# Kernel optimization log

Measured on AMD Instinct MI355X. Metric: run time of the kernel, lower is better.

## Reference

```python
import jax, jax.numpy as jnp
import numpy as np

DIM = 768
N_HEAD = 12
HEAD_DIM = 64
INNER = N_HEAD * HEAD_DIM
SCALE = HEAD_DIM ** -0.5


def setup_inputs() -> dict:
    key = jax.random.key(0)
    ks = jax.random.split(key, 12)
    B, Sf, St = 4, 2048, 2048
    from_tensor = jax.random.normal(ks[0], (B, Sf, DIM), dtype=jnp.float32)
    to_tensor = jax.random.normal(ks[1], (B, St, DIM), dtype=jnp.float32)
    attention_mask = jax.random.randint(ks[2], (B, Sf, St), 0, 2, dtype=jnp.int32)
    # Dense layers: kernel ~ RandomNormal (stddev 0.05, keras default), bias zeros
    def kern(k, fan_in, fan_out):
        return 0.05 * jax.random.normal(k, (fan_in, fan_out), dtype=jnp.float32)
    return {
        "from_tensor": from_tensor,
        "to_tensor": to_tensor,
        "attention_mask": attention_mask,
        "Wq": kern(ks[3], DIM, INNER), "bq": jnp.zeros((INNER,), jnp.float32),
        "Wk": kern(ks[4], DIM, INNER), "bk": jnp.zeros((INNER,), jnp.float32),
        "Wv": kern(ks[5], DIM, INNER), "bv": jnp.zeros((INNER,), jnp.float32),
        "Wo": kern(ks[6], INNER, DIM), "bo": jnp.zeros((DIM,), jnp.float32),
    }


def reference(from_tensor, to_tensor, attention_mask, Wq, bq, Wk, bk, Wv, bv, Wo, bo):
    B, Sf, _ = from_tensor.shape
    St = to_tensor.shape[1]
    # projections -> [B, S, n_head, head_dim] -> [B, n_head, S, head_dim]
    def split_heads(x, S):
        return x.reshape(B, S, N_HEAD, HEAD_DIM).transpose(0, 2, 1, 3)
    q = split_heads(from_tensor @ Wq + bq, Sf) * SCALE
    k = split_heads(to_tensor @ Wk + bk, St)
    v = split_heads(to_tensor @ Wv + bv, St)
    # scores [B, H, Sf, St]
    scores = jnp.einsum('bhik,bhjk->bhij', q, k)
    adder = (1.0 - attention_mask.astype(jnp.float32)) * -10000.0
    scores = scores + adder[:, None, :, :]
    probs = jax.nn.softmax(scores, axis=-1)
    out = jnp.einsum('bhij,bhjk->bhik', probs, v)  # [B, H, Sf, Dh]
    out = out.transpose(0, 2, 1, 3).reshape(B, Sf, INNER)
    return out @ Wo + bo
```

## Files before the change

### kernel.cpp

```cpp
#include <hip/hip_runtime.h>
#include <stdint.h>

#define DIM 768
#define NH 12
#define HD 64
#define BSZ 4
#define SEQ 2048
#define MROWS (BSZ*SEQ)

typedef __attribute__((ext_vector_type(8))) short v8s;
typedef __attribute__((ext_vector_type(4))) float v4f;
typedef __attribute__((ext_vector_type(8))) _Float16 v8h;
typedef __attribute__((ext_vector_type(2))) __fp16 v2fp;

__device__ __forceinline__ uint16_t f2bf(float x) {
  union { float f; uint32_t u; } v; v.f = x;
  uint32_t r = v.u + 0x7fffu + ((v.u >> 16) & 1u);
  return (uint16_t)(r >> 16);
}

#if __has_builtin(__builtin_amdgcn_cvt_pk_bf16_f32)
typedef __attribute__((ext_vector_type(2))) __bf16 v2bf;
__device__ __forceinline__ uint32_t pack_bf16(float a, float b) {
  union { v2bf v; uint32_t u; } c;
  c.v = __builtin_amdgcn_cvt_pk_bf16_f32(a, b);
  return c.u;
}
#else
__device__ __forceinline__ uint32_t pack_bf16(float a, float b) {
  return (uint32_t)f2bf(a) | ((uint32_t)f2bf(b) << 16);
}
#endif

__device__ __forceinline__ uint32_t pack_f16(float a, float b) {
#if __has_builtin(__builtin_amdgcn_cvt_pkrtz)
  union { v2fp h; uint32_t u; } c;
  c.h = __builtin_amdgcn_cvt_pkrtz(a, b);
  return c.u;
#else
  union { _Float16 h[2]; uint32_t u; } c;
  c.h[0] = (_Float16)a; c.h[1] = (_Float16)b; return c.u;
#endif
}

__device__ __forceinline__ float fexp2(float x) {
#if __has_builtin(__builtin_amdgcn_exp2f)
  return __builtin_amdgcn_exp2f(x);
#else
  return exp2f(x);
#endif
}

__device__ __forceinline__ unsigned long long spread4(uint32_t c) {
  unsigned long long x = c & 0xFFFFu;
  x = (x | (x << 24)) & 0x000000FF000000FFull;
  x = (x | (x << 12)) & 0x000F000F000F000Full;
  x = (x | (x << 6))  & 0x0303030303030303ull;
  x = (x | (x << 3))  & 0x1111111111111111ull;
  return x;
}

__device__ __forceinline__ void gl16(const void* g, void* l) {
  __builtin_amdgcn_global_load_lds(
      (const __attribute__((address_space(1))) unsigned int*)g,
      (__attribute__((address_space(3))) unsigned int*)l, 16, 0, 0);
}

__device__ __forceinline__ void pipe_sync() {
  asm volatile("s_waitcnt vmcnt(0)" ::: "memory");
  __builtin_amdgcn_s_barrier();
  __builtin_amdgcn_sched_barrier(0);
}

#define CVT_BLKS  12288
#define WT_BLKS   2304
#define MASK_BLKS 16384
__global__ __launch_bounds__(256) void prepass_kernel(
    const float* __restrict__ from_t, const float* __restrict__ to_t,
    uint16_t* __restrict__ Xf, uint16_t* __restrict__ Xt,
    const float* __restrict__ Wq, const float* __restrict__ Wk,
    const float* __restrict__ Wv, const float* __restrict__ Wo,
    uint16_t* __restrict__ WT,
    const int* __restrict__ maski, unsigned long long* __restrict__ Mbits)
{
  __shared__ float tile[32][33];
  int blk = blockIdx.x, tid = threadIdx.x;
  if (blk < CVT_BLKS) {
    int n4 = MROWS * DIM / 4;
    int i = blk * 256 + tid;
    const float* src = (i < n4) ? from_t : to_t;
    uint16_t* dst = (i < n4) ? Xf : Xt;
    int j = (i < n4) ? i : i - n4;
    float4 v = ((const float4*)src)[j];
    uint2 o;
    o.x = pack_bf16(v.x, v.y);
    o.y = pack_bf16(v.z, v.w);
    ((uint2*)dst)[j] = o;
  } else if (blk < CVT_BLKS + WT_BLKS) {
    int r = blk - CVT_BLKS;
    int z = r / 576, rem = r - z * 576;
    int by = rem / 24, bx = rem - by * 24;
    const float* src = (z==0) ? Wq : (z==1) ? Wk : (z==2) ? Wv : Wo;
    uint16_t* dst = WT + (size_t)z * DIM * DIM;
    int tx = tid & 31, ty = tid >> 5;
    int x  = bx * 32 + tx;
    int y0 = by * 32;
    for (int jj = ty; jj < 32; jj += 8)
      tile[jj][tx] = src[(size_t)(y0 + jj) * DIM + x];
    __syncthreads();
    int xo = y0 + tx;
    for (int jj = ty; jj < 32; jj += 8)
      dst[(size_t)(bx * 32 + jj) * DIM + xo] = f2bf(tile[tx][jj]);
  } else {
    int gtid = (blk - CVT_BLKS - WT_BLKS) * 256 + tid;
    int g = gtid >> 6;
    int lane = tid & 63;
    int b   = g >> 14;
    int q   = (g >> 3) & 2047;
    int ktb = (g & 7) * 4;
    size_t base = ((size_t)b * SEQ + q) * SEQ + (size_t)ktb * 64;
    int4 m = *(const int4*)&maski[base + (lane >> 4) * 64 + (lane & 15) * 4];
    unsigned long long b0 = __ballot(m.x != 0);
    unsigned long long b1 = __ballot(m.y != 0);
    unsigned long long b2 = __ballot(m.z != 0);
    unsigned long long b3 = __ballot(m.w != 0);
    int qd = lane >> 4, sh = qd * 16;
    unsigned long long word =  spread4((uint32_t)(b0 >> sh))
                            | (spread4((uint32_t)(b1 >> sh)) << 1)
                            | (spread4((uint32_t)(b2 >> sh)) << 2)
                            | (spread4((uint32_t)(b3 >> sh)) << 3);
    if ((lane & 15) == 0)
      Mbits[((size_t)b * 32 + ktb + qd) * SEQ + q] = word;
  }
}

__global__ __launch_bounds__(256) void gemm_kernel(
    const uint16_t* __restrict__ Xf, const uint16_t* __restrict__ Xt,
    const uint16_t* __restrict__ WT,
    const float* __restrict__ bq, const float* __restrict__ bk,
    const float* __restrict__ bv,
    uint16_t* __restrict__ Qw, uint16_t* __restrict__ Kw, uint16_t* __restrict__ Vw)
{
  __shared__ alignas(16) uint16_t As[2][128 * 32];
  __shared__ alignas(16) uint16_t Bs[2][128 * 32];
  int mode = blockIdx.z;
  const uint16_t* A = (mode == 0) ? Xf : Xt;
  const uint16_t* W = WT + (size_t)mode * DIM * DIM;
  const float* bias = (mode == 0) ? bq : (mode == 1) ? bk : bv;

  int m0 = blockIdx.x * 128, n0 = blockIdx.y * 128;
  int tid = threadIdx.x;
  int wave = tid >> 6, lane = tid & 63, lr = lane & 15, quad = lane >> 4;
  int wm = (wave >> 1) * 64, wn = (wave & 1) * 64;

  int seg = (lane & 3) ^ ((lane >> 3) & 3);
  const uint16_t* agl = A + (size_t)(m0 + wave * 32 + (lane >> 2)) * DIM + seg * 8;
  const uint16_t* bgl = W + (size_t)(n0 + wave * 32 + (lane >> 2)) * DIM + seg * 8;
  int lb = wave * 1024;
  int ck = (lr >> 1) & 3;

  v4f acc[4][4];
  v4f vz = {0.f, 0.f, 0.f, 0.f};
  #pragma unroll
  for (int i = 0; i < 4; i++)
    #pragma unroll
    for (int j = 0; j < 4; j++) acc[i][j] = vz;

  gl16(agl,            &As[0][lb]);
  gl16(agl + 16 * DIM, &As[0][lb + 512]);
  gl16(bgl,            &Bs[0][lb]);
  gl16(bgl + 16 * DIM, &Bs[0][lb + 512]);
  pipe_sync();

  int cur = 0;
  const int NT = DIM / 32;
  for (int t = 0; t < NT; ++t) {
    if (t + 1 < NT) {
      int kn = (t + 1) * 32;
      gl16(agl + kn,            &As[cur ^ 1][lb]);
      gl16(agl + kn + 16 * DIM, &As[cur ^ 1][lb + 512]);
      gl16(bgl + kn,            &Bs[cur ^ 1][lb]);
      gl16(bgl + kn + 16 * DIM, &Bs[cur ^ 1][lb + 512]);
    }
    v8s af[4], bfr[4];
    #pragma unroll
    for (int i = 0; i < 4; i++)
      af[i] = *(const v8s*)&As[cur][(wm + i * 16 + lr) * 32 + ((quad ^ ck) << 3)];
    #pragma unroll
    for (int j = 0; j < 4; j++)
      bfr[j] = *(const v8s*)&Bs[cur][(wn + j * 16 + lr) * 32 + ((quad ^ ck) << 3)];
    #pragma unroll
    for (int i = 0; i < 4; i++)
      #pragma unroll
      for (int j = 0; j < 4; j++)
        acc[i][j] = __builtin_amdgcn_mfma_f32_16x16x32_bf16(af[i], bfr[j], acc[i][j], 0, 0, 0);
    if (t + 1 < NT) pipe_sync();
    cur ^= 1;
  }

  float bj[4];
  #pragma unroll
  for (int j = 0; j < 4; j++) bj[j] = bias[n0 + wn + j * 16 + lr];

  if (mode == 2) {
    #pragma unroll
    for (int i = 0; i < 4; i++) {
      int m = m0 + wm + i * 16 + quad * 4;
      int b = m >> 11, s0 = m & 2047;
      int kk0 = s0 & 63;
      int pos = (kk0 >> 5) * 32 + ((kk0 >> 2) & 3) * 8 + ((kk0 >> 4) & 1) * 4;
      int chunk = pos >> 3, off = pos & 7;
      #pragma unroll
      for (int j = 0; j < 4; j++) {
        int n = n0 + wn + j * 16 + lr;
        int h = n >> 6, d = n & 63;
        uint2 pk;
        pk.x = pack_f16(acc[i][j][0] + bj[j], acc[i][j][1] + bj[j]);
        pk.y = pack_f16(acc[i][j][2] + bj[j], acc[i][j][3] + bj[j]);
        int idx = (s0 & ~63) + ((chunk ^ (d & 7)) << 3) + off;
        *(uint2*)&Vw[((size_t)(b * NH + h) * HD + d) * SEQ + idx] = pk;
      }
    }
  } else {
    uint16_t* Dst = (mode == 0) ? Qw : Kw;
    float scale = (mode == 0) ? 0.18033688f : 1.0f;
    #pragma unroll
    for (int i = 0; i < 4; i++) {
      int m = m0 + wm + i * 16 + quad * 4;
      int b = m >> 11, s0 = m & 2047;
      #pragma unroll
      for (int j = 0; j < 4; j++) {
        int n = n0 + wn + j * 16 + lr;
        int h = n >> 6, d = n & 63;
        #pragma unroll
        for (int r = 0; r < 4; r++) {
          float v = (acc[i][j][r] + bj[j]) * scale;
          int s = s0 + r;
          int dd = (mode == 1) ? ((((d >> 3) ^ (s & 7)) << 3) + (d & 7)) : d;
          Dst[((size_t)(b * NH + h) * SEQ + s) * HD + dd] = f2bf(v);
        }
      }
    }
  }
}

__global__ __launch_bounds__(256) void gemm64_kernel(
    const uint16_t* __restrict__ AO, const uint16_t* __restrict__ WT,
    const float* __restrict__ bo, float* __restrict__ Out)
{
  __shared__ alignas(16) uint16_t As[2][64 * 32];
  __shared__ alignas(16) uint16_t Bs[2][128 * 32];
  const uint16_t* W = WT + (size_t)3 * DIM * DIM;

  int m0 = blockIdx.x * 64, n0 = blockIdx.y * 128;
  int tid = threadIdx.x;
  int wave = tid >> 6, lane = tid & 63, lr = lane & 15, quad = lane >> 4;
  int wm = (wave >> 1) * 32, wn = (wave & 1) * 64;

  int seg = (lane & 3) ^ ((lane >> 3) & 3);
  const uint16_t* agl = AO + (size_t)(m0 + wave * 16 + (lane >> 2)) * DIM + seg * 8;
  const uint16_t* bgl = W  + (size_t)(n0 + wave * 32 + (lane >> 2)) * DIM + seg * 8;
  int lba = wave * 512;
  int lbb = wave * 1024;
  int ck = (lr >> 1) & 3;

  v4f acc[2][4];
  v4f vz = {0.f, 0.f, 0.f, 0.f};
  #pragma unroll
  for (int i = 0; i < 2; i++)
    #pragma unroll
    for (int j = 0; j < 4; j++) acc[i][j] = vz;

  gl16(agl,            &As[0][lba]);
  gl16(bgl,            &Bs[0][lbb]);
  gl16(bgl + 16 * DIM, &Bs[0][lbb + 512]);
  pipe_sync();

  int cur = 0;
  const int NT = DIM / 32;
  for (int t = 0; t < NT; ++t) {
    if (t + 1 < NT) {
      int kn = (t + 1) * 32;
      gl16(agl + kn,            &As[cur ^ 1][lba]);
      gl16(bgl + kn,            &Bs[cur ^ 1][lbb]);
      gl16(bgl + kn + 16 * DIM, &Bs[cur ^ 1][lbb + 512]);
    }
    v8s af[2], bfr[4];
    #pragma unroll
    for (int i = 0; i < 2; i++)
      af[i] = *(const v8s*)&As[cur][(wm + i * 16 + lr) * 32 + ((quad ^ ck) << 3)];
    #pragma unroll
    for (int j = 0; j < 4; j++)
      bfr[j] = *(const v8s*)&Bs[cur][(wn + j * 16 + lr) * 32 + ((quad ^ ck) << 3)];
    #pragma unroll
    for (int i = 0; i < 2; i++)
      #pragma unroll
      for (int j = 0; j < 4; j++)
        acc[i][j] = __builtin_amdgcn_mfma_f32_16x16x32_bf16(af[i], bfr[j], acc[i][j], 0, 0, 0);
    if (t + 1 < NT) pipe_sync();
    cur ^= 1;
  }

  float bj[4];
  #pragma unroll
  for (int j = 0; j < 4; j++) bj[j] = bo[n0 + wn + j * 16 + lr];

  #pragma unroll
  for (int i = 0; i < 2; i++) {
    int m = m0 + wm + i * 16 + quad * 4;
    #pragma unroll
    for (int j = 0; j < 4; j++) {
      int n = n0 + wn + j * 16 + lr;
      #pragma unroll
      for (int r = 0; r < 4; r++)
        Out[(size_t)(m + r) * DIM + n] = acc[i][j][r] + bj[j];
    }
  }
}

__global__ __launch_bounds__(256, 3) void flash_kernel(
    const uint16_t* __restrict__ Qg, const uint16_t* __restrict__ Kg,
    const uint16_t* __restrict__ Vg, const unsigned long long* __restrict__ Mb,
    uint16_t* __restrict__ AO)
{
  __shared__ alignas(16) uint16_t Ks[2][64 * 64];
  __shared__ alignas(16) uint16_t Vs[2][64 * 64];

  int tid = threadIdx.x, wave = tid >> 6, lane = tid & 63, lr = lane & 15, quad = lane >> 4;

  int d = blockIdx.x + (blockIdx.y << 4);
  int nid = (d & 7) * 96 + (d >> 3);
  int bh = nid >> 4;
  int q0 = (nid & 15) * 128;
  int b = bh / NH, h = bh - b * NH;

  const uint16_t* Qp = Qg + (size_t)bh * SEQ * HD;
  const uint16_t* Kp = Kg + (size_t)bh * SEQ * HD;
  const uint16_t* Vp = Vg + (size_t)bh * HD * SEQ;
  int qg0 = q0 + wave * 32 + lr;
  int qg1 = qg0 + 16;
  const unsigned long long* Mp0 = Mb + (size_t)b * 32 * SEQ + qg0;
  const unsigned long long* Mp1 = Mp0 + 16;

  int swk = lr & 7, sh0 = quad * 4;

  v8s qf0a = *(const v8s*)&Qp[(size_t)qg0 * HD + quad * 8];
  v8s qf0b = *(const v8s*)&Qp[(size_t)qg0 * HD + 32 + quad * 8];
  v8s qf1a = *(const v8s*)&Qp[(size_t)qg1 * HD + quad * 8];
  v8s qf1b = *(const v8s*)&Qp[(size_t)qg1 * HD + 32 + quad * 8];

  const uint16_t* kgl = Kp + ((size_t)(wave * 16 + (lane >> 3)) * HD + (lane & 7) * 8);
  const uint16_t* vgl = Vp + ((size_t)(wave * 16 + (lane >> 3)) * SEQ + (lane & 7) * 8);
  int lb = wave * 1024;

  v8h ones;
  #pragma unroll
  for (int i = 0; i < 8; i++) ones[i] = (_Float16)1.0f;

  v4f acc0[4], acc1[4], lacc0, lacc1;
  v4f vz = {0.f, 0.f, 0.f, 0.f};
  v4f m8 = {-8.f, -8.f, -8.f, -8.f};
  #pragma unroll
  for (int dt = 0; dt < 4; dt++) { acc0[dt] = vz; acc1[dt] = vz; }
  lacc0 = vz; lacc1 = vz;

  gl16(kgl,                   &Ks[0][lb]);
  gl16(kgl + (size_t)8 * HD,  &Ks[0][lb + 512]);
  gl16(vgl,                   &Vs[0][lb]);
  gl16(vgl + (size_t)8 * SEQ, &Vs[0][lb + 512]);
  unsigned long long mw0_cur = Mp0[0];
  unsigned long long mw1_cur = Mp1[0];
  __syncthreads();

  int cur = 0;
  const int NT = SEQ / 64;
  for (int it = 0; it < NT; ++it) {
    unsigned long long mw0_next = 0, mw1_next = 0;
    if (it + 1 < NT) {
      int kn = (it + 1) * 64;
      gl16(kgl + (size_t)kn * HD,       &Ks[cur ^ 1][lb]);
      gl16(kgl + (size_t)(kn + 8) * HD, &Ks[cur ^ 1][lb + 512]);
      gl16(vgl + kn,                    &Vs[cur ^ 1][lb]);
      gl16(vgl + kn + (size_t)8 * SEQ,  &Vs[cur ^ 1][lb + 512]);
      mw0_next = Mp0[(size_t)(it + 1) * SEQ];
      mw1_next = Mp1[(size_t)(it + 1) * SEQ];
    }

    uint32_t m0lo = (uint32_t)mw0_cur, m0hi = (uint32_t)(mw0_cur >> 32);
    uint32_t m1lo = (uint32_t)mw1_cur, m1hi = (uint32_t)(mw1_cur >> 32);
    v8h pf0[2], pf1[2];
    #pragma unroll
    for (int p = 0; p < 2; p++) {
      v4f sA0 = m8, sB0 = m8, sA1 = m8, sB1 = m8;
      __builtin_amdgcn_s_setprio(1);
      {
        int rowb = ((2 * p) * 16 + lr) << 6;
        v8s kf0 = *(const v8s*)&Ks[cur][rowb + ((quad ^ swk) << 3)];
        v8s kf1 = *(const v8s*)&Ks[cur][rowb + (((quad + 4) ^ swk) << 3)];
        sA0 = __builtin_amdgcn_mfma_f32_16x16x32_bf16(kf0, qf0a, sA0, 0, 0, 0);
        sA0 = __builtin_amdgcn_mfma_f32_16x16x32_bf16(kf1, qf0b, sA0, 0, 0, 0);
        sA1 = __builtin_amdgcn_mfma_f32_16x16x32_bf16(kf0, qf1a, sA1, 0, 0, 0);
        sA1 = __builtin_amdgcn_mfma_f32_16x16x32_bf16(kf1, qf1b, sA1, 0, 0, 0);
      }
      {
        int rowb = ((2 * p + 1) * 16 + lr) << 6;
        v8s kf0 = *(const v8s*)&Ks[cur][rowb + ((quad ^ swk) << 3)];
        v8s kf1 = *(const v8s*)&Ks[cur][rowb + (((quad + 4) ^ swk) << 3)];
        sB0 = __builtin_amdgcn_mfma_f32_16x16x32_bf16(kf0, qf0a, sB0, 0, 0, 0);
        sB0 = __builtin_amdgcn_mfma_f32_16x16x32_bf16(kf1, qf0b, sB0, 0, 0, 0);
        sB1 = __builtin_amdgcn_mfma_f32_16x16x32_bf16(kf0, qf1a, sB1, 0, 0, 0);
        sB1 = __builtin_amdgcn_mfma_f32_16x16x32_bf16(kf1, qf1b, sB1, 0, 0, 0);
      }
      __builtin_amdgcn_s_setprio(0);
      uint32_t w0 = p ? m0hi : m0lo, w1 = p ? m1hi : m1lo;
      uint32_t a0 = (w0 >> sh0) & 15u, b0 = (w0 >> (sh0 + 16)) & 15u;
      uint32_t a1 = (w1 >> sh0) & 15u, b1 = (w1 >> (sh0 + 16)) & 15u;
      float p0[8], p1[8];
      #pragma unroll
      for (int r = 0; r < 4; r++) {
        float e0a = fexp2(sA0[r]), e0b = fexp2(sB0[r]);
        float e1a = fexp2(sA1[r]), e1b = fexp2(sB1[r]);
        p0[r]     = (a0 & (1u << r)) ? e0a : 0.0f;
        p0[4 + r] = (b0 & (1u << r)) ? e0b : 0.0f;
        p1[r]     = (a1 & (1u << r)) ? e1a : 0.0f;
        p1[4 + r] = (b1 & (1u << r)) ? e1b : 0.0f;
      }
      union { uint4 u; v8h h; } c0, c1;
      c0.u.x = pack_f16(p0[0], p0[1]); c0.u.y = pack_f16(p0[2], p0[3]);
      c0.u.z = pack_f16(p0[4], p0[5]); c0.u.w = pack_f16(p0[6], p0[7]);
      c1.u.x = pack_f16(p1[0], p1[1]); c1.u.y = pack_f16(p1[2], p1[3]);
      c1.u.z = pack_f16(p1[4], p1[5]); c1.u.w = pack_f16(p1[6], p1[7]);
      pf0[p] = c0.h;
      pf1[p] = c1.h;
    }

    __builtin_amdgcn_s_setprio(1);
    #pragma unroll
    for (int dt = 0; dt < 4; dt++) {
      int rowb = (dt * 16 + lr) << 6;
      #pragma unroll
      for (int p = 0; p < 2; p++) {
        v8h vv = *(const v8h*)&Vs[cur][rowb + (((p * 4 + quad) ^ swk) << 3)];
        acc0[dt] = __builtin_amdgcn_mfma_f32_16x16x32_f16(vv, pf0[p], acc0[dt], 0, 0, 0);
        acc1[dt] = __builtin_amdgcn_mfma_f32_16x16x32_f16(vv, pf1[p], acc1[dt], 0, 0, 0);
      }
    }
    lacc0 = __builtin_amdgcn_mfma_f32_16x16x32_f16(ones, pf0[0], lacc0, 0, 0, 0);
    lacc0 = __builtin_amdgcn_mfma_f32_16x16x32_f16(ones, pf0[1], lacc0, 0, 0, 0);
    lacc1 = __builtin_amdgcn_mfma_f32_16x16x32_f16(ones, pf1[0], lacc1, 0, 0, 0);
    lacc1 = __builtin_amdgcn_mfma_f32_16x16x32_f16(ones, pf1[1], lacc1, 0, 0, 0);
    __builtin_amdgcn_s_setprio(0);

    __syncthreads();
    mw0_cur = mw0_next;
    mw1_cur = mw1_next;
    cur ^= 1;
  }

  float ri0 = 1.0f / lacc0[0];
  float ri1 = 1.0f / lacc1[0];

  #pragma unroll
  for (int dt = 0; dt < 4; dt++) {
    uint2 pk;
    pk.x = pack_bf16(acc0[dt][0] * ri0, acc0[dt][1] * ri0);
    pk.y = pack_bf16(acc0[dt][2] * ri0, acc0[dt][3] * ri0);
    *(uint2*)&AO[(size_t)(b * SEQ + qg0) * DIM + h * HD + dt * 16 + sh0] = pk;
    pk.x = pack_bf16(acc1[dt][0] * ri1, acc1[dt][1] * ri1);
    pk.y = pack_bf16(acc1[dt][2] * ri1, acc1[dt][3] * ri1);
    *(uint2*)&AO[(size_t)(b * SEQ + qg1) * DIM + h * HD + dt * 16 + sh0] = pk;
  }
}

extern "C" void kernel_launch(void* const* d_in, const int* in_sizes, int n_in,
                              void* d_out, int out_size, void* d_ws, size_t ws_size,
                              hipStream_t stream) {
  const float* from_t = (const float*)d_in[0];
  const float* to_t   = (const float*)d_in[1];
  const int*   maski  = (const int*)d_in[2];
  const float* Wq = (const float*)d_in[3];  const float* bq = (const float*)d_in[4];
  const float* Wk = (const float*)d_in[5];  const float* bk = (const float*)d_in[6];
  const float* Wv = (const float*)d_in[7];  const float* bv = (const float*)d_in[8];
  const float* Wo = (const float*)d_in[9];  const float* bo = (const float*)d_in[10];

  char* ws = (char*)d_ws;
  size_t off = 0;
  uint16_t* Xf = (uint16_t*)(ws + off); off += (size_t)MROWS * DIM * 2;
  uint16_t* Xt = (uint16_t*)(ws + off); off += (size_t)MROWS * DIM * 2;
  uint16_t* WT = (uint16_t*)(ws + off); off += (size_t)4 * DIM * DIM * 2;
  unsigned long long* Mbits = (unsigned long long*)(ws + off);
  off += (size_t)BSZ * 32 * SEQ * 8;
  uint16_t* Qw = (uint16_t*)(ws + off); off += (size_t)MROWS * DIM * 2;
  uint16_t* Kw = (uint16_t*)(ws + off); off += (size_t)MROWS * DIM * 2;
  uint16_t* Vw = (uint16_t*)(ws + off); off += (size_t)MROWS * DIM * 2;
  uint16_t* AO = (uint16_t*)(ws + off); off += (size_t)MROWS * DIM * 2;
  float* Out = (float*)d_out;

  prepass_kernel<<<CVT_BLKS + WT_BLKS + MASK_BLKS, 256, 0, stream>>>(
      from_t, to_t, Xf, Xt, Wq, Wk, Wv, Wo, WT, maski, Mbits);

  gemm_kernel<<<dim3(64, 6, 3), 256, 0, stream>>>(Xf, Xt, WT, bq, bk, bv,
                                                  Qw, Kw, Vw);
  flash_kernel<<<dim3(SEQ / 128, BSZ * NH), 256, 0, stream>>>(Qw, Kw, Vw, Mbits, AO);
  gemm64_kernel<<<dim3(128, 6), 256, 0, stream>>>(AO, WT, bo, Out);
}
```

Measured before the change: 304.6 us.

## Triple-buffer K/V tiles with prefetch distance two and manual vmcnt waits

Moves the flash attention loop from double to triple LDS buffering: each iteration issues async loads for the tile two steps ahead, waits with explicit s_waitcnt vmcnt(6) plus a raw s_barrier instead of __syncthreads, and unrolls by two so the mask words rotate between registers. The aim is to hide global load latency behind more compute and remove the full drain at each barrier. LDS per block grows from 32KB to 48KB, which may limit the three blocks per CU requested in launch bounds. The manual vmcnt counting also depends on exactly which memory ops are in flight.

```diff
diff --git a/kernel.cpp b/kernel.cpp
--- a/kernel.cpp
+++ b/kernel.cpp
@@ -318,13 +318,90 @@
   }
 }
 
+#define FLASH_TILE(CUR, M0LO, M0HI, M1LO, M1HI)                                   \
+  {                                                                               \
+    v8h pf0[2], pf1[2];                                                           \
+    _Pragma("unroll")                                                             \
+    for (int p = 0; p < 2; p++) {                                                 \
+      v4f sA0 = m8, sB0 = m8, sA1 = m8, sB1 = m8;                                 \
+      __builtin_amdgcn_s_setprio(1);                                              \
+      {                                                                           \
+        int rowb = ((2 * p) * 16 + lr) << 6;                                      \
+        v8s kf0 = *(const v8s*)&Ks[CUR][rowb + ((quad ^ swk) << 3)];              \
+        v8s kf1 = *(const v8s*)&Ks[CUR][rowb + (((quad + 4) ^ swk) << 3)];        \
+        sA0 = __builtin_amdgcn_mfma_f32_16x16x32_bf16(kf0, qf0a, sA0, 0, 0, 0);   \
+        sA0 = __builtin_amdgcn_mfma_f32_16x16x32_bf16(kf1, qf0b, sA0, 0, 0, 0);   \
+        sA1 = __builtin_amdgcn_mfma_f32_16x16x32_bf16(kf0, qf1a, sA1, 0, 0, 0);   \
+        sA1 = __builtin_amdgcn_mfma_f32_16x16x32_bf16(kf1, qf1b, sA1, 0, 0, 0);   \
+      }                                                                           \
+      {                                                                           \
+        int rowb = ((2 * p + 1) * 16 + lr) << 6;                                  \
+        v8s kf0 = *(const v8s*)&Ks[CUR][rowb + ((quad ^ swk) << 3)];              \
+        v8s kf1 = *(const v8s*)&Ks[CUR][rowb + (((quad + 4) ^ swk) << 3)];        \
+        sB0 = __builtin_amdgcn_mfma_f32_16x16x32_bf16(kf0, qf0a, sB0, 0, 0, 0);   \
+        sB0 = __builtin_amdgcn_mfma_f32_16x16x32_bf16(kf1, qf0b, sB0, 0, 0, 0);   \
+        sB1 = __builtin_amdgcn_mfma_f32_16x16x32_bf16(kf0, qf1a, sB1, 0, 0, 0);   \
+        sB1 = __builtin_amdgcn_mfma_f32_16x16x32_bf16(kf1, qf1b, sB1, 0, 0, 0);   \
+      }                                                                           \
+      __builtin_amdgcn_s_setprio(0);                                              \
+      uint32_t w0 = p ? (M0HI) : (M0LO), w1 = p ? (M1HI) : (M1LO);                \
+      uint32_t a0 = (w0 >> sh0) & 15u, b0 = (w0 >> (sh0 + 16)) & 15u;             \
+      uint32_t a1 = (w1 >> sh0) & 15u, b1 = (w1 >> (sh0 + 16)) & 15u;             \
+      float p0[8], p1[8];                                                         \
+      _Pragma("unroll")                                                           \
+      for (int r = 0; r < 4; r++) {                                               \
+        float e0a = fexp2(sA0[r]), e0b = fexp2(sB0[r]);                           \
+        float e1a = fexp2(sA1[r]), e1b = fexp2(sB1[r]);                           \
+        p0[r]     = (a0 & (1u << r)) ? e0a : 0.0f;                                \
+        p0[4 + r] = (b0 & (1u << r)) ? e0b : 0.0f;                                \
+        p1[r]     = (a1 & (1u << r)) ? e1a : 0.0f;                                \
+        p1[4 + r] = (b1 & (1u << r)) ? e1b : 0.0f;                                \
+      }                                                                           \
+      union { uint4 u; v8h h; } c0, c1;                                           \
+      c0.u.x = pack_f16(p0[0], p0[1]); c0.u.y = pack_f16(p0[2], p0[3]);           \
+      c0.u.z = pack_f16(p0[4], p0[5]); c0.u.w = pack_f16(p0[6], p0[7]);           \
+      c1.u.x = pack_f16(p1[0], p1[1]); c1.u.y = pack_f16(p1[2], p1[3]);           \
+      c1.u.z = pack_f16(p1[4], p1[5]); c1.u.w = pack_f16(p1[6], p1[7]);           \
+      pf0[p] = c0.h;                                                              \
+      pf1[p] = c1.h;                                                              \
+    }                                                                             \
+    __builtin_amdgcn_s_setprio(1);                                                \
+    _Pragma("unroll")                                                             \
+    for (int dt = 0; dt < 4; dt++) {                                              \
+      int rowb = (dt * 16 + lr) << 6;                                             \
+      _Pragma("unroll")                                                           \
+      for (int p = 0; p < 2; p++) {                                               \
+        v8h vv = *(const v8h*)&Vs[CUR][rowb + (((p * 4 + quad) ^ swk) << 3)];     \
+        acc0[dt] = __builtin_amdgcn_mfma_f32_16x16x32_f16(vv, pf0[p], acc0[dt], 0, 0, 0); \
+        acc1[dt] = __builtin_amdgcn_mfma_f32_16x16x32_f16(vv, pf1[p], acc1[dt], 0, 0, 0); \
+      }                                                                           \
+    }                                                                             \
+    lacc0 = __builtin_amdgcn_mfma_f32_16x16x32_f16(ones, pf0[0], lacc0, 0, 0, 0); \
+    lacc0 = __builtin_amdgcn_mfma_f32_16x16x32_f16(ones, pf0[1], lacc0, 0, 0, 0); \
+    lacc1 = __builtin_amdgcn_mfma_f32_16x16x32_f16(ones, pf1[0], lacc1, 0, 0, 0); \
+    lacc1 = __builtin_amdgcn_mfma_f32_16x16x32_f16(ones, pf1[1], lacc1, 0, 0, 0); \
+    __builtin_amdgcn_s_setprio(0);                                                \
+  }
+
+#define FLASH_STAGE(T, MW0, MW1)                                                  \
+  if ((T) + 2 < NT) {                                                             \
+    MW0 = Mp0[(size_t)((T) + 2) * SEQ];                                           \
+    MW1 = Mp1[(size_t)((T) + 2) * SEQ];                                           \
+    int kn = ((T) + 2) * 64;                                                      \
+    int nb = (cur == 0) ? 2 : cur - 1;                             \
+    gl16(kgl + (size_t)kn * HD,       &Ks[nb][lb]);                               \
+    gl16(kgl + (size_t)(kn + 8) * HD, &Ks[nb][lb + 512]);                         \
+    gl16(vgl + kn,                    &Vs[nb][lb]);                               \
+    gl16(vgl + kn + (size_t)8 * SEQ,  &Vs[nb][lb + 512]);                         \
+  }
+
 __global__ __launch_bounds__(256, 3) void flash_kernel(
     const uint16_t* __restrict__ Qg, const uint16_t* __restrict__ Kg,
     const uint16_t* __restrict__ Vg, const unsigned long long* __restrict__ Mb,
     uint16_t* __restrict__ AO)
 {
-  __shared__ alignas(16) uint16_t Ks[2][64 * 64];
-  __shared__ alignas(16) uint16_t Vs[2][64 * 64];
+  __shared__ alignas(16) uint16_t Ks[3][64 * 64];
+  __shared__ alignas(16) uint16_t Vs[3][64 * 64];
 
   int tid = threadIdx.x, wave = tid >> 6, lane = tid & 63, lr = lane & 15, quad = lane >> 4;
 
@@ -364,97 +441,46 @@
   for (int dt = 0; dt < 4; dt++) { acc0[dt] = vz; acc1[dt] = vz; }
   lacc0 = vz; lacc1 = vz;
 
-  gl16(kgl,                   &Ks[0][lb]);
-  gl16(kgl + (size_t)8 * HD,  &Ks[0][lb + 512]);
-  gl16(vgl,                   &Vs[0][lb]);
-  gl16(vgl + (size_t)8 * SEQ, &Vs[0][lb + 512]);
-  unsigned long long mw0_cur = Mp0[0];
-  unsigned long long mw1_cur = Mp1[0];
-  __syncthreads();
+  const int NT = SEQ / 64;
+
+  unsigned long long mwA0 = Mp0[0];
+  unsigned long long mwA1 = Mp1[0];
+  gl16(kgl,                    &Ks[0][lb]);
+  gl16(kgl + (size_t)8 * HD,   &Ks[0][lb + 512]);
+  gl16(vgl,                    &Vs[0][lb]);
+  gl16(vgl + (size_t)8 * SEQ,  &Vs[0][lb + 512]);
+  __builtin_amdgcn_sched_barrier(0);
+  unsigned long long mwB0 = Mp0[SEQ];
+  unsigned long long mwB1 = Mp1[SEQ];
+  gl16(kgl + (size_t)64 * HD,       &Ks[1][lb]);
+  gl16(kgl + (size_t)(64 + 8) * HD, &Ks[1][lb + 512]);
+  gl16(vgl + 64,                    &Vs[1][lb]);
+  gl16(vgl + 64 + (size_t)8 * SEQ,  &Vs[1][lb + 512]);
+  __builtin_amdgcn_sched_barrier(0);
 
   int cur = 0;
-  const int NT = SEQ / 64;
-  for (int it = 0; it < NT; ++it) {
-    unsigned long long mw0_next = 0, mw1_next = 0;
-    if (it + 1 < NT) {
-      int kn = (it + 1) * 64;
-      gl16(kgl + (size_t)kn * HD,       &Ks[cur ^ 1][lb]);
-      gl16(kgl + (size_t)(kn + 8) * HD, &Ks[cur ^ 1][lb + 512]);
-      gl16(vgl + kn,                    &Vs[cur ^ 1][lb]);
-      gl16(vgl + kn + (size_t)8 * SEQ,  &Vs[cur ^ 1][lb + 512]);
-      mw0_next = Mp0[(size_t)(it + 1) * SEQ];
-      mw1_next = Mp1[(size_t)(it + 1) * SEQ];
-    }
-
-    uint32_t m0lo = (uint32_t)mw0_cur, m0hi = (uint32_t)(mw0_cur >> 32);
-    uint32_t m1lo = (uint32_t)mw1_cur, m1hi = (uint32_t)(mw1_cur >> 32);
-    v8h pf0[2], pf1[2];
-    #pragma unroll
-    for (int p = 0; p < 2; p++) {
-      v4f sA0 = m8, sB0 = m8, sA1 = m8, sB1 = m8;
-      __builtin_amdgcn_s_setprio(1);
-      {
-        int rowb = ((2 * p) * 16 + lr) << 6;
-        v8s kf0 = *(const v8s*)&Ks[cur][rowb + ((quad ^ swk) << 3)];
-        v8s kf1 = *(const v8s*)&Ks[cur][rowb + (((quad + 4) ^ swk) << 3)];
-        sA0 = __builtin_amdgcn_mfma_f32_16x16x32_bf16(kf0, qf0a, sA0, 0, 0, 0);
-        sA0 = __builtin_amdgcn_mfma_f32_16x16x32_bf16(kf1, qf0b, sA0, 0, 0, 0);
-        sA1 = __builtin_amdgcn_mfma_f32_16x16x32_bf16(kf0, qf1a, sA1, 0, 0, 0);
-        sA1 = __builtin_amdgcn_mfma_f32_16x16x32_bf16(kf1, qf1b, sA1, 0, 0, 0);
-      }
-      {
-        int rowb = ((2 * p + 1) * 16 + lr) << 6;
-        v8s kf0 = *(const v8s*)&Ks[cur][rowb + ((quad ^ swk) << 3)];
-        v8s kf1 = *(const v8s*)&Ks[cur][rowb + (((quad + 4) ^ swk) << 3)];
-        sB0 = __builtin_amdgcn_mfma_f32_16x16x32_bf16(kf0, qf0a, sB0, 0, 0, 0);
-        sB0 = __builtin_amdgcn_mfma_f32_16x16x32_bf16(kf1, qf0b, sB0, 0, 0, 0);
-        sB1 = __builtin_amdgcn_mfma_f32_16x16x32_bf16(kf0, qf1a, sB1, 0, 0, 0);
-        sB1 = __builtin_amdgcn_mfma_f32_16x16x32_bf16(kf1, qf1b, sB1, 0, 0, 0);
-      }
-      __builtin_amdgcn_s_setprio(0);
-      uint32_t w0 = p ? m0hi : m0lo, w1 = p ? m1hi : m1lo;
-      uint32_t a0 = (w0 >> sh0) & 15u, b0 = (w0 >> (sh0 + 16)) & 15u;
-      uint32_t a1 = (w1 >> sh0) & 15u, b1 = (w1 >> (sh0 + 16)) & 15u;
-      float p0[8], p1[8];
-      #pragma unroll
-      for (int r = 0; r < 4; r++) {
-        float e0a = fexp2(sA0[r]), e0b = fexp2(sB0[r]);
-        float e1a = fexp2(sA1[r]), e1b = fexp2(sB1[r]);
-        p0[r]     = (a0 & (1u << r)) ? e0a : 0.0f;
-        p0[4 + r] = (b0 & (1u << r)) ? e0b : 0.0f;
-        p1[r]     = (a1 & (1u << r)) ? e1a : 0.0f;
-        p1[4 + r] = (b1 & (1u << r)) ? e1b : 0.0f;
-      }
-      union { uint4 u; v8h h; } c0, c1;
-      c0.u.x = pack_f16(p0[0], p0[1]); c0.u.y = pack_f16(p0[2], p0[3]);
-      c0.u.z = pack_f16(p0[4], p0[5]); c0.u.w = pack_f16(p0[6], p0[7]);
-      c1.u.x = pack_f16(p1[0], p1[1]); c1.u.y = pack_f16(p1[2], p1[3]);
-      c1.u.z = pack_f16(p1[4], p1[5]); c1.u.w = pack_f16(p1[6], p1[7]);
-      pf0[p] = c0.h;
-      pf1[p] = c1.h;
-    }
-
-    __builtin_amdgcn_s_setprio(1);
-    #pragma unroll
-    for (int dt = 0; dt < 4; dt++) {
-      int rowb = (dt * 16 + lr) << 6;
-      #pragma unroll
-      for (int p = 0; p < 2; p++) {
-        v8h vv = *(const v8h*)&Vs[cur][rowb + (((p * 4 + quad) ^ swk) << 3)];
-        acc0[dt] = __builtin_amdgcn_mfma_f32_16x16x32_f16(vv, pf0[p], acc0[dt], 0, 0, 0);
-        acc1[dt] = __builtin_amdgcn_mfma_f32_16x16x32_f16(vv, pf1[p], acc1[dt], 0, 0, 0);
-      }
-    }
-    lacc0 = __builtin_amdgcn_mfma_f32_16x16x32_f16(ones, pf0[0], lacc0, 0, 0, 0);
-    lacc0 = __builtin_amdgcn_mfma_f32_16x16x32_f16(ones, pf0[1], lacc0, 0, 0, 0);
-    lacc1 = __builtin_amdgcn_mfma_f32_16x16x32_f16(ones, pf1[0], lacc1, 0, 0, 0);
-    lacc1 = __builtin_amdgcn_mfma_f32_16x16x32_f16(ones, pf1[1], lacc1, 0, 0, 0);
-    __builtin_amdgcn_s_setprio(0);
-
-    __syncthreads();
-    mw0_cur = mw0_next;
-    mw1_cur = mw1_next;
-    cur ^= 1;
+  for (int t2 = 0; t2 < NT; t2 += 2) {
+    {
+      asm volatile("s_waitcnt vmcnt(6)" ::: "memory");
+      __builtin_amdgcn_s_barrier();
+      __builtin_amdgcn_sched_barrier(0);
+      uint32_t m0lo = (uint32_t)mwA0, m0hi = (uint32_t)(mwA0 >> 32);
+      uint32_t m1lo = (uint32_t)mwA1, m1hi = (uint32_t)(mwA1 >> 32);
+      FLASH_STAGE(t2, mwA0, mwA1);
+      FLASH_TILE(cur, m0lo, m0hi, m1lo, m1hi);
+      cur = (cur == 2) ? 0 : cur + 1;
+    }
+    {
+      if (t2 + 2 < NT) asm volatile("s_waitcnt vmcnt(6)" ::: "memory");
+      else             asm volatile("s_waitcnt vmcnt(0)" ::: "memory");
+      __builtin_amdgcn_s_barrier();
+      __builtin_amdgcn_sched_barrier(0);
+      uint32_t m0lo = (uint32_t)mwB0, m0hi = (uint32_t)(mwB0 >> 32);
+      uint32_t m1lo = (uint32_t)mwB1, m1hi = (uint32_t)(mwB1 >> 32);
+      FLASH_STAGE(t2 + 1, mwB0, mwB1);
+      FLASH_TILE(cur, m0lo, m0hi, m1lo, m1hi);
+      cur = (cur == 2) ? 0 : cur + 1;
+    }
   }
 
   float ri0 = 1.0f / lacc0[0];
```

Measured after the change: 304.2 us. About the same (-0.1%).
